# Kernel optimization log

Measured on AMD Instinct MI355X. Metric: run time of the kernel, lower is better.

## Reference

```python
import jax, jax.numpy as jnp
import numpy as np
import math

B, T, N, D = 2, 2048, 16, 128


def setup_inputs() -> dict:
    key = jax.random.key(0)
    ks = jax.random.split(key, 9)
    s = 1.0 / math.sqrt(D)
    return {
        "x": jax.random.normal(ks[0], (B, T, N, D), dtype=jnp.float32),
        "wq": jax.random.normal(ks[1], (D, D), dtype=jnp.float32) * s,
        "bq": jax.random.normal(ks[2], (D,), dtype=jnp.float32) * 0.02,
        "wk": jax.random.normal(ks[3], (D, D), dtype=jnp.float32) * s,
        "bk": jax.random.normal(ks[4], (D,), dtype=jnp.float32) * 0.02,
        "wv": jax.random.normal(ks[5], (D, D), dtype=jnp.float32) * s,
        "bv": jax.random.normal(ks[6], (D,), dtype=jnp.float32) * 0.02,
        "wp": jax.random.normal(ks[7], (D, D), dtype=jnp.float32) * s,
        "bp": jax.random.normal(ks[8], (D,), dtype=jnp.float32) * 0.02,
    }


def reference(x, wq, bq, wk, bk, wv, bv, wp, bp):
    # x: (B, T, N, D); per-head Linear projections (torch y = x @ W.T + b)
    d = x.shape[-1]
    q = jnp.einsum("btnd,ed->btne", x, wq) + bq  # (B,T,N,D)
    k = jnp.einsum("btnd,ed->btne", x, wk) + bk
    v = jnp.einsum("btnd,ed->btne", x, wv) + bv
    scale = 1.0 / jnp.sqrt(jnp.asarray(d, dtype=x.dtype))
    # scores: (B, N, T, T)
    scores = jnp.einsum("btnd,bsnd->bnts", q, k) * scale
    t = scores.shape[-1]
    causal = jnp.tril(jnp.ones((t, t), dtype=bool))  # (T,T)
    scores = jnp.where(causal[None, None], scores, jnp.asarray(-jnp.inf, scores.dtype))
    w = jax.nn.softmax(scores, axis=-1)
    att = jnp.einsum("bnts,bsnd->btnd", w, v)  # (B,T,N,D)
    out = jnp.einsum("btnd,ed->btne", att, wp) + bp
    return out
```

## Files before the change

### kernel.cpp

```cpp
#include <hip/hip_runtime.h>
#include <cmath>

#define BB 2
#define TT 2048
#define NN 16
#define DD 128
#define NROWS (BB*TT*NN)
#define PLANE (TT*DD)
#define KP 132
#define VP 68

typedef unsigned short u16;
typedef unsigned int   u32;
typedef __attribute__((ext_vector_type(8)))  short s8v;
typedef __attribute__((ext_vector_type(16))) float vf16;

__device__ u16 g_Q [(size_t)NROWS * DD];
__device__ u16 g_K [(size_t)NROWS * DD];
__device__ u16 g_V [(size_t)NROWS * DD];
__device__ u16 g_VT[(size_t)NROWS * DD];

__device__ __forceinline__ u16 f2bf(float f) {
    return (u16)((__float_as_uint(f) + 0x8000u) >> 16);
}
__device__ __forceinline__ u32 pk2(float a, float b) {
    return ((__float_as_uint(a) + 0x8000u) >> 16)
         | ((__float_as_uint(b) + 0x8000u) & 0xFFFF0000u);
}
__device__ __forceinline__ void st8(u16* p, const float4& a, const float4& b) {
    uint2 lo, hi;
    lo.x = pk2(a.x, a.y); lo.y = pk2(a.z, a.w);
    hi.x = pk2(b.x, b.y); hi.y = pk2(b.z, b.w);
    *(uint2*)p       = lo;
    *(uint2*)(p + 4) = hi;
}
__device__ __forceinline__ s8v ld8(const u16* p) {
    short4 a = *(const short4*)p;
    short4 b = *(const short4*)(p + 4);
    return (s8v){a.x, a.y, a.z, a.w, b.x, b.y, b.z, b.w};
}

__device__ __forceinline__ void bar_lds()
{
    asm volatile("s_waitcnt lgkmcnt(0)" ::: "memory");
    __builtin_amdgcn_sched_barrier(0);
    __builtin_amdgcn_s_barrier();
    __builtin_amdgcn_sched_barrier(0);
}

__global__ __launch_bounds__(256)
void qkv_proj_kernel(const float* __restrict__ x,
                     const float* __restrict__ Wq, const float* __restrict__ Bq,
                     const float* __restrict__ Wk, const float* __restrict__ Bk,
                     const float* __restrict__ Wv, const float* __restrict__ Bv)
{
    __shared__ u16 Xs[128*KP];
    __shared__ u16 Ws[128*KP];

    const int t  = threadIdx.x;
    const int r0 = blockIdx.x * 128;
    const float4* xsrc = (const float4*)(x + (size_t)r0*DD);

    #pragma unroll
    for (int it = 0; it < 8; ++it) {
        int i = t + 256*it;
        int e = i >> 4, c8 = i & 15;
        st8(&Xs[e*KP + c8*8], xsrc[2*i], xsrc[2*i + 1]);
    }
    #pragma unroll
    for (int it = 0; it < 8; ++it) {
        int i = t + 256*it;
        int e = i >> 4, c8 = i & 15;
        st8(&Ws[e*KP + c8*8], ((const float4*)Wq)[2*i], ((const float4*)Wq)[2*i + 1]);
    }
    __syncthreads();

    const int w   = t >> 6;
    const int l31 = t & 31;
    const int q2  = (t >> 5) & 1;

    s8v af[8];
    #pragma unroll
    for (int s = 0; s < 8; ++s)
        af[s] = ld8(&Xs[(w*32 + l31)*KP + s*16 + q2*8]);

    #pragma unroll
    for (int wsel = 0; wsel < 3; ++wsel) {
        const float* Bi = (wsel == 0) ? Bq : (wsel == 1) ? Bk : Bv;
        u16*         Ot = (wsel == 0) ? g_Q : (wsel == 1) ? g_K : g_V;

        vf16 acc[4];
        #pragma unroll
        for (int et = 0; et < 4; ++et)
            #pragma unroll
            for (int i = 0; i < 16; ++i) acc[et][i] = 0.f;

        #pragma unroll
        for (int s = 0; s < 8; ++s) {
            #pragma unroll
            for (int et = 0; et < 4; ++et) {
                s8v bf = ld8(&Ws[(et*32 + l31)*KP + s*16 + q2*8]);
                acc[et] = __builtin_amdgcn_mfma_f32_32x32x16_bf16(af[s], bf, acc[et], 0, 0, 0);
            }
        }

        float bb[4];
        #pragma unroll
        for (int et = 0; et < 4; ++et) bb[et] = Bi[et*32 + l31];

        #pragma unroll
        for (int r = 0; r < 16; ++r) {
            int rl = (r & 3) + 8*(r >> 2) + 4*q2;
            int rg = r0 + w*32 + rl;
            int b = rg >> 15, rem = rg & 32767;
            int tt = rem >> 4, n = rem & 15;
            size_t orow = (size_t)((b*NN + n)*TT + tt) * DD;
            #pragma unroll
            for (int et = 0; et < 4; ++et) {
                float ov = acc[et][r] + bb[et];
                if (wsel == 0) ov *= 0.12752053685940512f;
                Ot[orow + et*32 + l31] = f2bf(ov);
            }
        }

        if (wsel < 2) {
            const float* Wn = (wsel == 0) ? Wk : Wv;
            __syncthreads();
            #pragma unroll
            for (int it = 0; it < 8; ++it) {
                int i = t + 256*it;
                int e = i >> 4, c8 = i & 15;
                st8(&Ws[e*KP + c8*8], ((const float4*)Wn)[2*i], ((const float4*)Wn)[2*i + 1]);
            }
            __syncthreads();
        }
    }
}

__global__ __launch_bounds__(256)
void out_proj_kernel(const float* __restrict__ W, const float* __restrict__ Bi,
                     float* __restrict__ out)
{
    __shared__ u16 Ws[128*KP];

    const int t  = threadIdx.x;
    const int r0 = blockIdx.x * 128;

    #pragma unroll
    for (int it = 0; it < 8; ++it) {
        int i = t + 256*it;
        int e = i >> 4, c8 = i & 15;
        st8(&Ws[e*KP + c8*8], ((const float4*)W)[2*i], ((const float4*)W)[2*i + 1]);
    }

    const int w   = t >> 6;
    const int l31 = t & 31;
    const int q2  = (t >> 5) & 1;

    s8v af[8];
    {
        const u16* src = g_Q + (size_t)(r0 + w*32 + l31)*DD;
        #pragma unroll
        for (int s = 0; s < 8; ++s)
            af[s] = *(const s8v*)&src[s*16 + q2*8];
    }
    __syncthreads();

    vf16 acc[4];
    #pragma unroll
    for (int et = 0; et < 4; ++et)
        #pragma unroll
        for (int i = 0; i < 16; ++i) acc[et][i] = 0.f;

    #pragma unroll
    for (int s = 0; s < 8; ++s) {
        #pragma unroll
        for (int et = 0; et < 4; ++et) {
            s8v bf = ld8(&Ws[(et*32 + l31)*KP + s*16 + q2*8]);
            acc[et] = __builtin_amdgcn_mfma_f32_32x32x16_bf16(af[s], bf, acc[et], 0, 0, 0);
        }
    }

    float bb[4];
    #pragma unroll
    for (int et = 0; et < 4; ++et) bb[et] = Bi[et*32 + l31];

    #pragma unroll
    for (int r = 0; r < 16; ++r) {
        int rl = (r & 3) + 8*(r >> 2) + 4*q2;
        int rg = r0 + w*32 + rl;
        int b = rg >> 15, rem = rg & 32767;
        int n = rem >> 11, tt = rem & 2047;
        size_t orow = (size_t)((b*TT + tt)*NN + n) * DD;
        #pragma unroll
        for (int et = 0; et < 4; ++et)
            out[orow + et*32 + l31] = acc[et][r] + bb[et];
    }
}

__global__ __launch_bounds__(256)
void vtrans_kernel()
{
    __shared__ u16 L[64*KP];

    const int t   = threadIdx.x;
    const int blk = blockIdx.x;
    const int pl  = blk >> 5;
    const int tt0 = (blk & 31) * 64;
    const size_t plane = (size_t)pl * PLANE;

    #pragma unroll
    for (int c = 0; c < 4; ++c) {
        int j = t + 256*c;
        int row = j >> 4, c16 = j & 15;
        uint4 v = *(const uint4*)&g_V[plane + (size_t)(tt0 + row)*DD + c16*8];
        *(uint4*)&L[row*KP + c16*8] = v;
    }
    __syncthreads();
    #pragma unroll
    for (int c = 0; c < 4; ++c) {
        int j = t + 256*c;
        int d = j >> 3, tc = j & 7;
        u16 e[8];
        #pragma unroll
        for (int i = 0; i < 8; ++i) e[i] = L[(tc*8 + i)*KP + d];
        uint4 pkv;
        pkv.x = (u32)e[0] | ((u32)e[1] << 16);
        pkv.y = (u32)e[2] | ((u32)e[3] << 16);
        pkv.z = (u32)e[4] | ((u32)e[5] << 16);
        pkv.w = (u32)e[6] | ((u32)e[7] << 16);
        *(uint4*)&g_VT[plane + (size_t)d*TT + tt0 + tc*8] = pkv;
    }
}

__global__ __launch_bounds__(256, 2)
void attn_kernel()
{
    __shared__ u16 Ks[2][64*KP];
    __shared__ u16 Vt[2][128*VP];

    const int t   = threadIdx.x;
    const int grp = blockIdx.x >> 5;
    const int bn  = blockIdx.x & 31;
    const int qt  = (grp < 8) ? (15 - grp) : (grp - 8);
    const int q0  = qt * 128;
    const size_t plane = (size_t)bn * PLANE;
    const u16* Kg = g_K  + plane;
    const u16* Vg = g_VT + plane;

    const int w      = t >> 6;
    const int lane   = t & 63;
    const int lane31 = lane & 31;
    const int q2     = lane >> 5;
    const int qband  = q0 + 32*w;
    const int qrow   = qband + lane31;

    s8v qf[8];
    {
        const u16* Qg = g_Q + plane + (size_t)qrow * DD;
        #pragma unroll
        for (int s = 0; s < 8; ++s)
            qf[s] = *(const s8v*)&Qg[s*16 + q2*8];
    }

    vf16 accO[4];
    #pragma unroll
    for (int dt = 0; dt < 4; ++dt)
        #pragma unroll
        for (int i = 0; i < 16; ++i) accO[dt][i] = 0.f;

    float lrow = 0.f;
    const int nkt = 2*qt + 2;

    uint4 pk[4], pv[4];

    auto LOADT = [&](int kt) {
        const u16* K2 = Kg + (size_t)(kt*64)*DD;
        const u16* V2 = Vg + kt*64;
        #pragma unroll
        for (int c = 0; c < 4; ++c) {
            int j = t + 256*c;
            int kr = j >> 4, kc = j & 15;
            pk[c] = *(const uint4*)&K2[kr*DD + kc*8];
            int vr = j >> 3, vc = j & 7;
            pv[c] = *(const uint4*)&V2[(size_t)vr*TT + vc*8];
        }
    };
    auto STORET = [&](int buf) {
        #pragma unroll
        for (int c = 0; c < 4; ++c) {
            int j = t + 256*c;
            int kr = j >> 4, kc = j & 15;
            uint2 a, b;
            a.x = pk[c].x; a.y = pk[c].y; b.x = pk[c].z; b.y = pk[c].w;
            *(uint2*)&Ks[buf][kr*KP + kc*8]     = a;
            *(uint2*)&Ks[buf][kr*KP + kc*8 + 4] = b;
            int vr = j >> 3, vc = j & 7;
            a.x = pv[c].x; a.y = pv[c].y; b.x = pv[c].z; b.y = pv[c].w;
            *(uint2*)&Vt[buf][vr*VP + vc*8]     = a;
            *(uint2*)&Vt[buf][vr*VP + vc*8 + 4] = b;
        }
    };

    LOADT(0);
    STORET(0);
    LOADT(1);

    for (int kt = 0; kt < nkt; ++kt) {
        const int k0 = kt*64;
        const int cb = kt & 1;
        bar_lds();

        if (kt + 1 < nkt) {
            STORET(cb ^ 1);
            if (kt + 2 < nkt) LOADT(kt + 2);
        }

        if (k0 <= qband + 31) {
            const u16* Kb = Ks[cb];
            const u16* Vb = Vt[cb];

            vf16 accS[2];
            #pragma unroll
            for (int kk = 0; kk < 2; ++kk)
                #pragma unroll
                for (int i = 0; i < 16; ++i) accS[kk][i] = 0.f;
            __builtin_amdgcn_s_setprio(1);
            #pragma unroll
            for (int s = 0; s < 8; ++s) {
                #pragma unroll
                for (int kk = 0; kk < 2; ++kk) {
                    s8v a = ld8(&Kb[(kk*32 + lane31)*KP + s*16 + q2*8]);
                    accS[kk] = __builtin_amdgcn_mfma_f32_32x32x16_bf16(a, qf[s], accS[kk], 0, 0, 0);
                }
            }
            __builtin_amdgcn_s_setprio(0);

            float p[2][16];
            const bool tail = (k0 + 63 > qband);
            #pragma unroll
            for (int kk = 0; kk < 2; ++kk)
                #pragma unroll
                for (int r = 0; r < 16; ++r) {
                    float sv = accS[kk][r];
                    if (tail) {
                        int keyg = k0 + kk*32 + (r & 3) + 8*(r >> 2) + 4*q2;
                        if (keyg > qrow) sv = -INFINITY;
                    }
                    p[kk][r] = sv;
                }

            float ls0 = 0.f, ls1 = 0.f;
            #pragma unroll
            for (int r = 0; r < 16; ++r) {
                float e0 = __builtin_amdgcn_exp2f(p[0][r] - 16.f);
                float e1 = __builtin_amdgcn_exp2f(p[1][r] - 16.f);
                p[0][r] = e0; p[1][r] = e1;
                ls0 += e0; ls1 += e1;
            }
            float ls = ls0 + ls1;
            ls += __shfl_xor(ls, 32);
            lrow += ls;

            s8v pf[4];
            #pragma unroll
            for (int tau = 0; tau < 4; ++tau) {
                int kk = tau >> 1, rb = (tau & 1)*8;
                s8v v;
                #pragma unroll
                for (int j = 0; j < 8; ++j)
                    v[j] = (short)(__float_as_uint(p[kk][rb + j]) >> 16);
                pf[tau] = v;
            }

            __builtin_amdgcn_s_setprio(1);
            #pragma unroll
            for (int dt = 0; dt < 4; ++dt) {
                const u16* vp = &Vb[(dt*32 + lane31)*VP];
                #pragma unroll
                for (int tau = 0; tau < 4; ++tau) {
                    const u16* q = vp + 16*tau + 4*q2;
                    short4 lo = *(const short4*)q;
                    short4 hi = *(const short4*)(q + 8);
                    s8v bvv = {lo.x, lo.y, lo.z, lo.w, hi.x, hi.y, hi.z, hi.w};
                    accO[dt] = __builtin_amdgcn_mfma_f32_32x32x16_bf16(pf[tau], bvv, accO[dt], 0, 0, 0);
                }
            }
            __builtin_amdgcn_s_setprio(0);
        }
    }

    float inv = 1.0f / lrow;
    #pragma unroll
    for (int r = 0; r < 16; ++r) {
        int rl = (r & 3) + 8*(r >> 2) + 4*q2;
        float ir = __shfl(inv, rl);
        u16* op = g_Q + plane + (size_t)(qband + rl)*DD;
        #pragma unroll
        for (int dt = 0; dt < 4; ++dt)
            op[dt*32 + lane31] = f2bf(accO[dt][r] * ir);
    }
}

extern "C" void kernel_launch(void* const* d_in, const int* in_sizes, int n_in,
                              void* d_out, int out_size, void* d_ws, size_t ws_size,
                              hipStream_t stream)
{
    const float* x  = (const float*)d_in[0];
    const float* wq = (const float*)d_in[1];
    const float* bq = (const float*)d_in[2];
    const float* wk = (const float*)d_in[3];
    const float* bk = (const float*)d_in[4];
    const float* wv = (const float*)d_in[5];
    const float* bv = (const float*)d_in[6];
    const float* wp = (const float*)d_in[7];
    const float* bp = (const float*)d_in[8];
    float* out = (float*)d_out;
    (void)d_ws; (void)ws_size;

    qkv_proj_kernel<<<dim3(NROWS/128), dim3(256), 0, stream>>>(
        x, wq, bq, wk, bk, wv, bv);
    vtrans_kernel<<<dim3(BB*NN*(TT/64)), dim3(256), 0, stream>>>();
    attn_kernel<<<dim3(BB*NN*(TT/128)), dim3(256), 0, stream>>>();
    out_proj_kernel<<<dim3(NROWS/128), dim3(256), 0, stream>>>(wp, bp, out);
}
```

Baseline: 189.7 us.

## Fuse V transpose into QKV projection and output projection into attention

The QKV projection kernel now tiles by (batch, head, 128-token block), so each block writes head-major Q/K directly and transposes V through shared memory to write V^T. This removes the separate transpose kernel and the intermediate g_V buffer. The attention kernel's epilogue stages the normalized output tile and Wp in shared memory and performs the output projection in place, dropping the out_proj kernel and the round trip of attention output through global memory. The cost is strided x reads in the projection, and extra LDS traffic and registers in the attention epilogue.

```diff
diff --git a/kernel.cpp b/kernel.cpp
--- a/kernel.cpp
+++ b/kernel.cpp
@@ -9,6 +9,7 @@
 #define PLANE (TT*DD)
 #define KP 132
 #define VP 68
+#define TP 129
 
 typedef unsigned short u16;
 typedef unsigned int   u32;
@@ -17,7 +18,6 @@
 
 __device__ u16 g_Q [(size_t)NROWS * DD];
 __device__ u16 g_K [(size_t)NROWS * DD];
-__device__ u16 g_V [(size_t)NROWS * DD];
 __device__ u16 g_VT[(size_t)NROWS * DD];
 
 __device__ __forceinline__ u16 f2bf(float f) {
@@ -57,15 +57,17 @@
     __shared__ u16 Xs[128*KP];
     __shared__ u16 Ws[128*KP];
 
-    const int t  = threadIdx.x;
-    const int r0 = blockIdx.x * 128;
-    const float4* xsrc = (const float4*)(x + (size_t)r0*DD);
+    const int t    = threadIdx.x;
+    const int bnp  = blockIdx.x >> 4;
+    const int tt0  = (blockIdx.x & 15) * 128;
+    const size_t xrow0 = ((size_t)((bnp >> 4)*TT + tt0)*NN + (bnp & 15)) * DD;
 
     #pragma unroll
     for (int it = 0; it < 8; ++it) {
         int i = t + 256*it;
         int e = i >> 4, c8 = i & 15;
-        st8(&Xs[e*KP + c8*8], xsrc[2*i], xsrc[2*i + 1]);
+        const float* xp = x + xrow0 + (size_t)e*(NN*DD) + c8*8;
+        st8(&Xs[e*KP + c8*8], *(const float4*)xp, *(const float4*)(xp + 4));
     }
     #pragma unroll
     for (int it = 0; it < 8; ++it) {
@@ -87,7 +89,6 @@
     #pragma unroll
     for (int wsel = 0; wsel < 3; ++wsel) {
         const float* Bi = (wsel == 0) ? Bq : (wsel == 1) ? Bk : Bv;
-        u16*         Ot = (wsel == 0) ? g_Q : (wsel == 1) ? g_K : g_V;
 
         vf16 acc[4];
         #pragma unroll
@@ -108,22 +109,19 @@
         #pragma unroll
         for (int et = 0; et < 4; ++et) bb[et] = Bi[et*32 + l31];
 
-        #pragma unroll
-        for (int r = 0; r < 16; ++r) {
-            int rl = (r & 3) + 8*(r >> 2) + 4*q2;
-            int rg = r0 + w*32 + rl;
-            int b = rg >> 15, rem = rg & 32767;
-            int tt = rem >> 4, n = rem & 15;
-            size_t orow = (size_t)((b*NN + n)*TT + tt) * DD;
-            #pragma unroll
-            for (int et = 0; et < 4; ++et) {
-                float ov = acc[et][r] + bb[et];
-                if (wsel == 0) ov *= 0.12752053685940512f;
-                Ot[orow + et*32 + l31] = f2bf(ov);
-            }
-        }
-
         if (wsel < 2) {
+            u16* Ot = (wsel == 0) ? g_Q : g_K;
+            #pragma unroll
+            for (int r = 0; r < 16; ++r) {
+                int rl = (r & 3) + 8*(r >> 2) + 4*q2;
+                size_t orow = (size_t)bnp*PLANE + (size_t)(tt0 + w*32 + rl)*DD;
+                #pragma unroll
+                for (int et = 0; et < 4; ++et) {
+                    float ov = acc[et][r] + bb[et];
+                    if (wsel == 0) ov *= 0.12752053685940512f;
+                    Ot[orow + et*32 + l31] = f2bf(ov);
+                }
+            }
             const float* Wn = (wsel == 0) ? Wk : Wv;
             __syncthreads();
             #pragma unroll
@@ -133,108 +131,39 @@
                 st8(&Ws[e*KP + c8*8], ((const float4*)Wn)[2*i], ((const float4*)Wn)[2*i + 1]);
             }
             __syncthreads();
-        }
-    }
-}
-
-__global__ __launch_bounds__(256)
-void out_proj_kernel(const float* __restrict__ W, const float* __restrict__ Bi,
-                     float* __restrict__ out)
-{
-    __shared__ u16 Ws[128*KP];
-
-    const int t  = threadIdx.x;
-    const int r0 = blockIdx.x * 128;
-
-    #pragma unroll
-    for (int it = 0; it < 8; ++it) {
-        int i = t + 256*it;
-        int e = i >> 4, c8 = i & 15;
-        st8(&Ws[e*KP + c8*8], ((const float4*)W)[2*i], ((const float4*)W)[2*i + 1]);
-    }
-
-    const int w   = t >> 6;
-    const int l31 = t & 31;
-    const int q2  = (t >> 5) & 1;
-
-    s8v af[8];
-    {
-        const u16* src = g_Q + (size_t)(r0 + w*32 + l31)*DD;
-        #pragma unroll
-        for (int s = 0; s < 8; ++s)
-            af[s] = *(const s8v*)&src[s*16 + q2*8];
-    }
-    __syncthreads();
-
-    vf16 acc[4];
-    #pragma unroll
-    for (int et = 0; et < 4; ++et)
-        #pragma unroll
-        for (int i = 0; i < 16; ++i) acc[et][i] = 0.f;
-
-    #pragma unroll
-    for (int s = 0; s < 8; ++s) {
-        #pragma unroll
-        for (int et = 0; et < 4; ++et) {
-            s8v bf = ld8(&Ws[(et*32 + l31)*KP + s*16 + q2*8]);
-            acc[et] = __builtin_amdgcn_mfma_f32_32x32x16_bf16(af[s], bf, acc[et], 0, 0, 0);
-        }
-    }
-
-    float bb[4];
-    #pragma unroll
-    for (int et = 0; et < 4; ++et) bb[et] = Bi[et*32 + l31];
-
-    #pragma unroll
-    for (int r = 0; r < 16; ++r) {
-        int rl = (r & 3) + 8*(r >> 2) + 4*q2;
-        int rg = r0 + w*32 + rl;
-        int b = rg >> 15, rem = rg & 32767;
-        int n = rem >> 11, tt = rem & 2047;
-        size_t orow = (size_t)((b*TT + tt)*NN + n) * DD;
-        #pragma unroll
-        for (int et = 0; et < 4; ++et)
-            out[orow + et*32 + l31] = acc[et][r] + bb[et];
-    }
-}
-
-__global__ __launch_bounds__(256)
-void vtrans_kernel()
-{
-    __shared__ u16 L[64*KP];
-
-    const int t   = threadIdx.x;
-    const int blk = blockIdx.x;
-    const int pl  = blk >> 5;
-    const int tt0 = (blk & 31) * 64;
-    const size_t plane = (size_t)pl * PLANE;
-
-    #pragma unroll
-    for (int c = 0; c < 4; ++c) {
-        int j = t + 256*c;
-        int row = j >> 4, c16 = j & 15;
-        uint4 v = *(const uint4*)&g_V[plane + (size_t)(tt0 + row)*DD + c16*8];
-        *(uint4*)&L[row*KP + c16*8] = v;
-    }
-    __syncthreads();
-    #pragma unroll
-    for (int c = 0; c < 4; ++c) {
-        int j = t + 256*c;
-        int d = j >> 3, tc = j & 7;
-        u16 e[8];
-        #pragma unroll
-        for (int i = 0; i < 8; ++i) e[i] = L[(tc*8 + i)*KP + d];
-        uint4 pkv;
-        pkv.x = (u32)e[0] | ((u32)e[1] << 16);
-        pkv.y = (u32)e[2] | ((u32)e[3] << 16);
-        pkv.z = (u32)e[4] | ((u32)e[5] << 16);
-        pkv.w = (u32)e[6] | ((u32)e[7] << 16);
-        *(uint4*)&g_VT[plane + (size_t)d*TT + tt0 + tc*8] = pkv;
+        } else {
+            u16* Xt = (u16*)Xs;
+            #pragma unroll
+            for (int r = 0; r < 16; ++r) {
+                int rl = (r & 3) + 8*(r >> 2) + 4*q2;
+                int row = w*32 + rl;
+                #pragma unroll
+                for (int et = 0; et < 4; ++et)
+                    Xt[row*TP + et*32 + l31] = f2bf(acc[et][r] + bb[et]);
+            }
+            __syncthreads();
+            const size_t vbase = (size_t)bnp*PLANE + tt0;
+            #pragma unroll
+            for (int c = 0; c < 8; ++c) {
+                int idx = t + 256*c;
+                int d = idx >> 4, tc = idx & 15;
+                u16 e8[8];
+                #pragma unroll
+                for (int i = 0; i < 8; ++i) e8[i] = Xt[(tc*8 + i)*TP + d];
+                uint4 pkv;
+                pkv.x = (u32)e8[0] | ((u32)e8[1] << 16);
+                pkv.y = (u32)e8[2] | ((u32)e8[3] << 16);
+                pkv.z = (u32)e8[4] | ((u32)e8[5] << 16);
+                pkv.w = (u32)e8[6] | ((u32)e8[7] << 16);
+                *(uint4*)&g_VT[vbase + (size_t)d*TT + tc*8] = pkv;
+            }
+        }
     }
 }
 
 __global__ __launch_bounds__(256, 2)
-void attn_kernel()
+void attn_kernel(const float* __restrict__ Wp, const float* __restrict__ Bp,
+                 float* __restrict__ out)
 {
     __shared__ u16 Ks[2][64*KP];
     __shared__ u16 Vt[2][128*VP];
@@ -390,15 +319,65 @@
         }
     }
 
-    float inv = 1.0f / lrow;
-    #pragma unroll
-    for (int r = 0; r < 16; ++r) {
-        int rl = (r & 3) + 8*(r >> 2) + 4*q2;
-        float ir = __shfl(inv, rl);
-        u16* op = g_Q + plane + (size_t)(qband + rl)*DD;
-        #pragma unroll
-        for (int dt = 0; dt < 4; ++dt)
-            op[dt*32 + lane31] = f2bf(accO[dt][r] * ir);
+    bar_lds();
+    u16* Os  = &Ks[0][0];
+    u16* Wps = &Vt[0][0];
+
+    {
+        float inv = 1.0f / lrow;
+        #pragma unroll
+        for (int r = 0; r < 16; ++r) {
+            int rl = (r & 3) + 8*(r >> 2) + 4*q2;
+            float ir = __shfl(inv, rl);
+            u16* op = &Os[(32*w + rl)*KP];
+            #pragma unroll
+            for (int dt = 0; dt < 4; ++dt)
+                op[dt*32 + lane31] = f2bf(accO[dt][r] * ir);
+        }
+    }
+    #pragma unroll
+    for (int it = 0; it < 8; ++it) {
+        int i = t + 256*it;
+        int e = i >> 4, c8 = i & 15;
+        st8(&Wps[e*KP + c8*8], ((const float4*)Wp)[2*i], ((const float4*)Wp)[2*i + 1]);
+    }
+    bar_lds();
+
+    {
+        s8v af[8];
+        #pragma unroll
+        for (int s = 0; s < 8; ++s)
+            af[s] = ld8(&Os[(w*32 + lane31)*KP + s*16 + q2*8]);
+
+        vf16 acc[4];
+        #pragma unroll
+        for (int et = 0; et < 4; ++et)
+            #pragma unroll
+            for (int i = 0; i < 16; ++i) acc[et][i] = 0.f;
+
+        #pragma unroll
+        for (int s = 0; s < 8; ++s) {
+            #pragma unroll
+            for (int et = 0; et < 4; ++et) {
+                s8v bf = ld8(&Wps[(et*32 + lane31)*KP + s*16 + q2*8]);
+                acc[et] = __builtin_amdgcn_mfma_f32_32x32x16_bf16(af[s], bf, acc[et], 0, 0, 0);
+            }
+        }
+
+        float bb[4];
+        #pragma unroll
+        for (int et = 0; et < 4; ++et) bb[et] = Bp[et*32 + lane31];
+
+        const int b = bn >> 4, n = bn & 15;
+        #pragma unroll
+        for (int r = 0; r < 16; ++r) {
+            int rl = (r & 3) + 8*(r >> 2) + 4*q2;
+            int qg = q0 + w*32 + rl;
+            size_t orow = ((size_t)(b*TT + qg)*NN + n) * DD;
+            #pragma unroll
+            for (int et = 0; et < 4; ++et)
+                out[orow + et*32 + lane31] = acc[et][r] + bb[et];
+        }
     }
 }
 
@@ -420,7 +399,5 @@
 
     qkv_proj_kernel<<<dim3(NROWS/128), dim3(256), 0, stream>>>(
         x, wq, bq, wk, bk, wv, bv);
-    vtrans_kernel<<<dim3(BB*NN*(TT/64)), dim3(256), 0, stream>>>();
-    attn_kernel<<<dim3(BB*NN*(TT/128)), dim3(256), 0, stream>>>();
-    out_proj_kernel<<<dim3(NROWS/128), dim3(256), 0, stream>>>(wp, bp, out);
-}
+    attn_kernel<<<dim3(BB*NN*(TT/128)), dim3(256), 0, stream>>>(wp, bp, out);
+}
```

Measured after the change: 172.5 us. -9.0%, faster.
